# Optimization experiments

Measured on AMD Instinct MI355X. Metric: run time of the kernel, lower is better.

## Reference

```python
import jax, jax.numpy as jnp
import numpy as np

NUM_NODES = 10000   # nodes per graph (softmax axis)
N_HEADS = 8
IN_CHANNELS = 32
NUM_GRAPHS = 64
TOTAL_NODES = NUM_NODES * NUM_GRAPHS


def setup_inputs() -> dict:
    key = jax.random.key(0)
    k_x, k_b, k_att = jax.random.split(key, 3)
    x = jax.random.normal(k_x, (TOTAL_NODES, IN_CHANNELS), dtype=jnp.float32)
    batch = jnp.sort(jax.random.randint(k_b, (TOTAL_NODES,), 0, NUM_GRAPHS)).astype(jnp.int64)
    att = jax.random.normal(k_att, (N_HEADS, NUM_NODES), dtype=jnp.float32)
    return {"x": x, "batch": batch, "att": att, "num_graphs": NUM_GRAPHS}


def reference(x, batch, att, num_graphs):
    # x: [N, C], batch: [N], att: [H, M]; N == M * num_graphs
    B = int(num_graphs)
    w = jax.nn.softmax(att, axis=1)          # [H, M] softmax over per-graph node slots
    w_full = jnp.tile(w, (1, B))             # [H, N] tiled per graph (repeat(1,B).view(-1,1))
    # per-head weighted scatter-add pooling keyed by batch id
    pooled = jax.vmap(
        lambda wh: jax.ops.segment_sum(x * wh[:, None], batch, num_segments=B)
    )(w_full)                                # [H, B, C]
    # torch.cat(pools, dim=-1): head-major blocks along feature axis
    return pooled.transpose(1, 0, 2).reshape(B, -1)  # [B, H*C]
```

## Files before the change

### kernel.cpp

```cpp
#include <hip/hip_runtime.h>
#include <math.h>

#define H 8
#define C 32
#define HC 256
#define KSL 32
#define PB 16

__device__ __forceinline__ float wred_sum(float v) {
#pragma unroll
    for (int o = 32; o; o >>= 1) v += __shfl_xor(v, o, 64);
    return v;
}
__device__ __forceinline__ float4 red4_no(float4 v) {
#pragma unroll
    for (int o = 8; o < 64; o <<= 1) {
        v.x += __shfl_xor(v.x, o, 64);
        v.y += __shfl_xor(v.y, o, 64);
        v.z += __shfl_xor(v.z, o, 64);
        v.w += __shfl_xor(v.w, o, 64);
    }
    return v;
}

__global__ __launch_bounds__(256) void expsum_kernel(
        const float* __restrict__ att, float* __restrict__ partials, int M) {
    const int h = blockIdx.x / PB;
    const int b = blockIdx.x % PB;
    const int s0 = (int)(((long)M * b) / PB);
    const int s1 = (int)(((long)M * (b + 1)) / PB);
    const float* __restrict__ row = att + (size_t)h * M;
    __shared__ float red[4];
    float s = 0.f;
    for (int i = s0 + threadIdx.x; i < s1; i += 256) s += __expf(row[i]);
    s = wred_sum(s);
    if ((threadIdx.x & 63) == 0) red[threadIdx.x >> 6] = s;
    __syncthreads();
    if (threadIdx.x == 0)
        partials[h * PB + b] = red[0] + red[1] + red[2] + red[3];
}

__global__ __launch_bounds__(256) void prep_kernel(
        const float* __restrict__ att, const int* __restrict__ batch,
        const float* __restrict__ partials, float* __restrict__ wtabT,
        int* __restrict__ segend, int M, int Ntot, int tb) {
    if ((int)blockIdx.x < tb) {
        __shared__ float sinv[H];
        if (threadIdx.x < H) {
            float s = 0.f;
#pragma unroll
            for (int k = 0; k < PB; ++k) s += partials[threadIdx.x * PB + k];
            sinv[threadIdx.x] = 1.0f / s;
        }
        __syncthreads();
        const int idx = blockIdx.x * 256 + threadIdx.x;
        if (idx < H * M) {
            const int hh = idx & (H - 1);
            const int mm = idx >> 3;
            wtabT[idx] = __expf(att[(size_t)hh * M + mm]) * sinv[hh];
        }
    } else {
        const int idx = ((int)blockIdx.x - tb) * 256 + threadIdx.x;
        if (idx < Ntot) {
            const int b = batch[idx];
            if (idx == Ntot - 1 || batch[idx + 1] != b) segend[b] = idx + 1;
        }
    }
}

#define FMA8(XV, W0, W1)                                              \
    a0.x = fmaf(XV.x, W0.x, a0.x); a0.y = fmaf(XV.y, W0.x, a0.y);     \
    a0.z = fmaf(XV.z, W0.x, a0.z); a0.w = fmaf(XV.w, W0.x, a0.w);     \
    a1.x = fmaf(XV.x, W0.y, a1.x); a1.y = fmaf(XV.y, W0.y, a1.y);     \
    a1.z = fmaf(XV.z, W0.y, a1.z); a1.w = fmaf(XV.w, W0.y, a1.w);     \
    a2.x = fmaf(XV.x, W0.z, a2.x); a2.y = fmaf(XV.y, W0.z, a2.y);     \
    a2.z = fmaf(XV.z, W0.z, a2.z); a2.w = fmaf(XV.w, W0.z, a2.w);     \
    a3.x = fmaf(XV.x, W0.w, a3.x); a3.y = fmaf(XV.y, W0.w, a3.y);     \
    a3.z = fmaf(XV.z, W0.w, a3.z); a3.w = fmaf(XV.w, W0.w, a3.w);     \
    a4.x = fmaf(XV.x, W1.x, a4.x); a4.y = fmaf(XV.y, W1.x, a4.y);     \
    a4.z = fmaf(XV.z, W1.x, a4.z); a4.w = fmaf(XV.w, W1.x, a4.w);     \
    a5.x = fmaf(XV.x, W1.y, a5.x); a5.y = fmaf(XV.y, W1.y, a5.y);     \
    a5.z = fmaf(XV.z, W1.y, a5.z); a5.w = fmaf(XV.w, W1.y, a5.w);     \
    a6.x = fmaf(XV.x, W1.z, a6.x); a6.y = fmaf(XV.y, W1.z, a6.y);     \
    a6.z = fmaf(XV.z, W1.z, a6.z); a6.w = fmaf(XV.w, W1.z, a6.w);     \
    a7.x = fmaf(XV.x, W1.w, a7.x); a7.y = fmaf(XV.y, W1.w, a7.y);     \
    a7.z = fmaf(XV.z, W1.w, a7.z); a7.w = fmaf(XV.w, W1.w, a7.w);

__global__ __launch_bounds__(256, 5) void poolA_kernel(
        const float* __restrict__ x, const float* __restrict__ wtabT,
        const int* __restrict__ segend, float* __restrict__ psum,
        int M, int Ntot) {
    const int g  = blockIdx.x >> 5;
    const int k  = blockIdx.x & (KSL - 1);
    const int wv = threadIdx.x >> 6;
    const int lane = threadIdx.x & 63;
    const int cg = lane & 7;
    const int no = lane >> 3;
    const int c  = cg << 2;

    const int s0 = (g == 0) ? 0 : segend[g - 1];
    const int s1 = segend[g];
    const int L  = s1 - s0;
    const int sb = s0 + (int)(((long)L * k) >> 5);
    const int sl = (s0 + (int)(((long)L * (k + 1)) >> 5)) - sb;
    int       n    = sb + (sl * wv) / 4;
    const int nEnd = sb + (sl * (wv + 1)) / 4;

    float4 a0 = {0,0,0,0}, a1 = {0,0,0,0}, a2 = {0,0,0,0}, a3 = {0,0,0,0};
    float4 a4 = {0,0,0,0}, a5 = {0,0,0,0}, a6 = {0,0,0,0}, a7 = {0,0,0,0};

    int m = n % M;
    while (n < nEnd) {
        const int run = min(nEnd - n, M - m);
        const float* xb = x + (size_t)(n + no) * C + c;
        const float* wb = wtabT + ((size_t)(m + no) << 3);
        const int full = run & ~7;
        int i = 0;
#pragma unroll 2
        for (; i < full; i += 8) {
            const float4 xv  = *(const float4*)(xb + (size_t)i * C);
            const float4 wv0 = *(const float4*)(wb + (size_t)i * 8);
            const float4 wv1 = *(const float4*)(wb + (size_t)i * 8 + 4);
            FMA8(xv, wv0, wv1)
        }
        const int rem = run - full;
        if (rem) {
            const int off = (no < rem) ? no : 0;
            const float4 xv = *(const float4*)(x + (size_t)(n + i + off) * C + c);
            float4 wv0 = {0,0,0,0}, wv1 = {0,0,0,0};
            if (no < rem) {
                const float* wb2 = wtabT + ((size_t)(m + i + no) << 3);
                wv0 = *(const float4*)(wb2);
                wv1 = *(const float4*)(wb2 + 4);
            }
            FMA8(xv, wv0, wv1)
        }
        n += run;
        m += run;
        if (m >= M) m = 0;
    }

    a0 = red4_no(a0); a1 = red4_no(a1); a2 = red4_no(a2); a3 = red4_no(a3);
    a4 = red4_no(a4); a5 = red4_no(a5); a6 = red4_no(a6); a7 = red4_no(a7);

    __shared__ float4 sacc[4][H][8];
    if (no == 0) {
        sacc[wv][0][cg] = a0; sacc[wv][1][cg] = a1;
        sacc[wv][2][cg] = a2; sacc[wv][3][cg] = a3;
        sacc[wv][4][cg] = a4; sacc[wv][5][cg] = a5;
        sacc[wv][6][cg] = a6; sacc[wv][7][cg] = a7;
    }
    __syncthreads();
    if (wv == 0) {
        const int hh = lane >> 3;
        const int cc = lane & 7;
        float4 s  = sacc[0][hh][cc];
        float4 t1 = sacc[1][hh][cc];
        float4 t2 = sacc[2][hh][cc];
        float4 t3 = sacc[3][hh][cc];
        s.x += t1.x + t2.x + t3.x;
        s.y += t1.y + t2.y + t3.y;
        s.z += t1.z + t2.z + t3.z;
        s.w += t1.w + t2.w + t3.w;
        float* o = psum + ((size_t)blockIdx.x << 8) + (hh << 5) + (cc << 2);
        *(float4*)o = s;
    }
}

__global__ __launch_bounds__(256) void reduceB_kernel(
        const float* __restrict__ psum, float* __restrict__ out) {
    const int g = blockIdx.x;
    const int i = threadIdx.x;
    const float* p = psum + ((size_t)g << 13) + i;
    float s = 0.f;
#pragma unroll
    for (int k = 0; k < KSL; ++k) s += p[(size_t)k << 8];
    out[(g << 8) + i] = s;
}

extern "C" void kernel_launch(void* const* d_in, const int* in_sizes, int n_in,
                              void* d_out, int out_size, void* d_ws, size_t ws_size,
                              hipStream_t stream) {
    const float* x     = (const float*)d_in[0];
    const int*   batch = (const int*)d_in[1];
    const float* att   = (const float*)d_in[2];
    float*       out   = (float*)d_out;

    const int Ntot = in_sizes[0] / C;
    const int M    = in_sizes[2] / H;
    const int B    = out_size / HC;

    float* partials = (float*)d_ws;
    int*   segend   = (int*)((char*)d_ws + 1024);
    float* wtabT    = (float*)((char*)d_ws + 4096);
    const size_t ps_off = (4096 + (size_t)H * M * sizeof(float) + 255) & ~(size_t)255;
    float* psum     = (float*)((char*)d_ws + ps_off);

    expsum_kernel<<<H * PB, 256, 0, stream>>>(att, partials, M);

    const int tb = (H * M + 255) / 256;
    const int sblocks = (Ntot + 255) / 256;
    prep_kernel<<<tb + sblocks, 256, 0, stream>>>(att, batch, partials, wtabT,
                                                  segend, M, Ntot, tb);

    poolA_kernel<<<B * KSL, 256, 0, stream>>>(x, wtabT, segend, psum, M, Ntot);

    reduceB_kernel<<<B, 256, 0, stream>>>(psum, out);
}
```

Before: 33.56 us.

## Defer softmax normalization to final reduce and merge expsum into prep kernel

The pooling weights are stored as unnormalized exponentials, and the per-head 1/sum scale is applied in the final reduction kernel. This lets the exp-sum partial computation run as extra blocks inside the prep kernel rather than as a separate launch that had to finish first. The aim is to remove one kernel launch and its serialization point. Each reduce block now redundantly sums the partials, and unnormalized exponentials could overflow for large attention values.

```diff
diff --git a/kernel.cpp b/kernel.cpp
--- a/kernel.cpp
+++ b/kernel.cpp
@@ -23,48 +23,39 @@
     return v;
 }
 
-__global__ __launch_bounds__(256) void expsum_kernel(
-        const float* __restrict__ att, float* __restrict__ partials, int M) {
-    const int h = blockIdx.x / PB;
-    const int b = blockIdx.x % PB;
-    const int s0 = (int)(((long)M * b) / PB);
-    const int s1 = (int)(((long)M * (b + 1)) / PB);
-    const float* __restrict__ row = att + (size_t)h * M;
-    __shared__ float red[4];
-    float s = 0.f;
-    for (int i = s0 + threadIdx.x; i < s1; i += 256) s += __expf(row[i]);
-    s = wred_sum(s);
-    if ((threadIdx.x & 63) == 0) red[threadIdx.x >> 6] = s;
-    __syncthreads();
-    if (threadIdx.x == 0)
-        partials[h * PB + b] = red[0] + red[1] + red[2] + red[3];
-}
-
 __global__ __launch_bounds__(256) void prep_kernel(
         const float* __restrict__ att, const int* __restrict__ batch,
-        const float* __restrict__ partials, float* __restrict__ wtabT,
-        int* __restrict__ segend, int M, int Ntot, int tb) {
-    if ((int)blockIdx.x < tb) {
-        __shared__ float sinv[H];
-        if (threadIdx.x < H) {
-            float s = 0.f;
-#pragma unroll
-            for (int k = 0; k < PB; ++k) s += partials[threadIdx.x * PB + k];
-            sinv[threadIdx.x] = 1.0f / s;
-        }
-        __syncthreads();
-        const int idx = blockIdx.x * 256 + threadIdx.x;
+        float* __restrict__ wtabT, int* __restrict__ segend,
+        float* __restrict__ partials, int M, int Ntot, int tb, int sb) {
+    const int bid = blockIdx.x;
+    if (bid < tb) {
+        const int idx = bid * 256 + threadIdx.x;
         if (idx < H * M) {
             const int hh = idx & (H - 1);
             const int mm = idx >> 3;
-            wtabT[idx] = __expf(att[(size_t)hh * M + mm]) * sinv[hh];
-        }
-    } else {
-        const int idx = ((int)blockIdx.x - tb) * 256 + threadIdx.x;
+            wtabT[idx] = __expf(att[(size_t)hh * M + mm]);
+        }
+    } else if (bid < tb + sb) {
+        const int idx = (bid - tb) * 256 + threadIdx.x;
         if (idx < Ntot) {
             const int b = batch[idx];
             if (idx == Ntot - 1 || batch[idx + 1] != b) segend[b] = idx + 1;
         }
+    } else {
+        const int pbid = bid - tb - sb;
+        const int h = pbid / PB;
+        const int p = pbid % PB;
+        const int s0 = (int)(((long)M * p) / PB);
+        const int s1 = (int)(((long)M * (p + 1)) / PB);
+        const float* __restrict__ row = att + (size_t)h * M;
+        __shared__ float red[4];
+        float s = 0.f;
+        for (int i = s0 + threadIdx.x; i < s1; i += 256) s += __expf(row[i]);
+        s = wred_sum(s);
+        if ((threadIdx.x & 63) == 0) red[threadIdx.x >> 6] = s;
+        __syncthreads();
+        if (threadIdx.x == 0)
+            partials[h * PB + p] = red[0] + red[1] + red[2] + red[3];
     }
 }
 
@@ -168,14 +159,23 @@
 }
 
 __global__ __launch_bounds__(256) void reduceB_kernel(
-        const float* __restrict__ psum, float* __restrict__ out) {
+        const float* __restrict__ psum, const float* __restrict__ partials,
+        float* __restrict__ out) {
+    __shared__ float sinv[H];
+    if (threadIdx.x < H) {
+        float s = 0.f;
+#pragma unroll
+        for (int k = 0; k < PB; ++k) s += partials[threadIdx.x * PB + k];
+        sinv[threadIdx.x] = 1.0f / s;
+    }
+    __syncthreads();
     const int g = blockIdx.x;
     const int i = threadIdx.x;
     const float* p = psum + ((size_t)g << 13) + i;
     float s = 0.f;
 #pragma unroll
     for (int k = 0; k < KSL; ++k) s += p[(size_t)k << 8];
-    out[(g << 8) + i] = s;
+    out[(g << 8) + i] = s * sinv[i >> 5];
 }
 
 extern "C" void kernel_launch(void* const* d_in, const int* in_sizes, int n_in,
@@ -196,14 +196,12 @@
     const size_t ps_off = (4096 + (size_t)H * M * sizeof(float) + 255) & ~(size_t)255;
     float* psum     = (float*)((char*)d_ws + ps_off);
 
-    expsum_kernel<<<H * PB, 256, 0, stream>>>(att, partials, M);
-
     const int tb = (H * M + 255) / 256;
     const int sblocks = (Ntot + 255) / 256;
-    prep_kernel<<<tb + sblocks, 256, 0, stream>>>(att, batch, partials, wtabT,
-                                                  segend, M, Ntot, tb);
+    prep_kernel<<<tb + sblocks + H * PB, 256, 0, stream>>>(
+        att, batch, wtabT, segend, partials, M, Ntot, tb, sblocks);
 
     poolA_kernel<<<B * KSL, 256, 0, stream>>>(x, wtabT, segend, psum, M, Ntot);
 
-    reduceB_kernel<<<B, 256, 0, stream>>>(psum, out);
-}
+    reduceB_kernel<<<B, 256, 0, stream>>>(psum, partials, out);
+}
```

Measured after the change: 31.15 us. -7.2%, faster.
